# Performance work log

Hardware: AMD Instinct MI355X
Metric: run time of the kernel (lower is better)

The kernel has to match this reference:

```python
import jax, jax.numpy as jnp
import numpy as np
from jax import lax

V, E, H, T, S = 100000, 256, 512, 9, 4096
HH = H // 2
START, STOP = 7, 8
NEG = -10000.0


def setup_inputs() -> dict:
    key = jax.random.key(0)
    ks = jax.random.split(key, 16)
    def n(k, shape, scale=0.1):
        return jax.random.normal(k, shape, jnp.float32) * scale
    sentence = jax.random.randint(ks[0], (S,), 0, V)
    embed = n(ks[1], (V, E), 1.0)
    w_ih_f = n(ks[2], (4 * HH, E)); w_hh_f = n(ks[3], (4 * HH, HH))
    b_ih_f = n(ks[4], (4 * HH,));   b_hh_f = n(ks[5], (4 * HH,))
    w_ih_b = n(ks[6], (4 * HH, E)); w_hh_b = n(ks[7], (4 * HH, HH))
    b_ih_b = n(ks[8], (4 * HH,));   b_hh_b = n(ks[9], (4 * HH,))
    h0 = n(ks[10], (2, HH), 1.0)  # init_hidden: randn (2,1,HH), batch squeezed
    c0 = n(ks[11], (2, HH), 1.0)
    W_out = n(ks[12], (T, H)); b_out = n(ks[13], (T,))
    transitions = jax.random.normal(ks[14], (T, T), jnp.float32)
    transitions = transitions.at[START, :].set(NEG).at[:, STOP].set(NEG)
    return dict(sentence=sentence, embed=embed,
                w_ih_f=w_ih_f, w_hh_f=w_hh_f, b_ih_f=b_ih_f, b_hh_f=b_hh_f,
                w_ih_b=w_ih_b, w_hh_b=w_hh_b, b_ih_b=b_ih_b, b_hh_b=b_hh_b,
                h0=h0, c0=c0, W_out=W_out, b_out=b_out, transitions=transitions)


def _lstm_dir(x_gates, h0, c0, w_hh):
    # x_gates: [S, 4*HH] = x @ w_ih.T + b_ih + b_hh (precomputed input part)
    def step(carry, xg):
        h, c = carry
        g = xg + h @ w_hh.T
        i, f, gg, o = jnp.split(g, 4)  # torch gate order: i, f, g, o
        i = jax.nn.sigmoid(i); f = jax.nn.sigmoid(f)
        gg = jnp.tanh(gg);     o = jax.nn.sigmoid(o)
        c = f * c + i * gg
        h = o * jnp.tanh(c)
        return (h, c), h
    _, hs = lax.scan(step, (h0, c0), x_gates)
    return hs  # [S, HH]


def reference(sentence, embed, w_ih_f, w_hh_f, b_ih_f, b_hh_f,
              w_ih_b, w_hh_b, b_ih_b, b_hh_b, h0, c0, W_out, b_out, transitions):
    x = embed[sentence]  # [S, E]
    # bidirectional LSTM, batch=1
    hf = _lstm_dir(x @ w_ih_f.T + b_ih_f + b_hh_f, h0[0], c0[0], w_hh_f)
    hb = _lstm_dir((x @ w_ih_b.T + b_ih_b + b_hh_b)[::-1], h0[1], c0[1], w_hh_b)[::-1]
    lstm_out = jnp.concatenate([hf, hb], axis=-1)          # [S, H]
    frames = lstm_out @ W_out.T + b_out                     # [S, T] emission scores

    # Viterbi-style decode (faithful: alpha updated by logsumexp, backpointers by argmax)
    alpha0 = jnp.full((T,), NEG, jnp.float32).at[START].set(0.0)
    def vstep(alpha, frame):
        smat = alpha[:, None] + frame[None, :] + transitions  # [T, T]
        bp = jnp.argmax(smat, axis=0)
        return jax.nn.logsumexp(smat, axis=0), bp
    alpha, bps = lax.scan(vstep, alpha0, frames)            # bps: [S, T]

    final = alpha + transitions[:, STOP]                     # [T]
    best = jnp.argmax(final)
    score = jax.nn.logsumexp(final)

    # backtrack over bps[1:] in reverse
    def bstep(tag, bp):
        nt = bp[tag]
        return nt, nt
    _, path_rev = lax.scan(bstep, best, bps[1:][::-1])
    tag_seq = jnp.concatenate([path_rev[::-1], best[None]])  # [S]
    return score, tag_seq
```

## Files before the change

kernel.cpp:

```cpp
#include <hip/hip_runtime.h>
#include <hip/hip_bf16.h>

#define SEQ   4096
#define EMB   256
#define HHID  256
#define G4    1024
#define NT    9
#define TSTART 7
#define TSTOP  8
#define NEGV  (-10000.0f)
#define POISON 0xAAAAAAAAu

#define WS_XG_F   0u
#define WS_XG_B   16777216u
#define WS_HF     33554432u
#define WS_HB     37748736u
#define WS_FRAMES 41943040u

__global__ __launch_bounds__(256) void xgate_kernel(
    const int* __restrict__ sentence, const float* __restrict__ embed,
    const float* __restrict__ w_ih_f, const float* __restrict__ b_ih_f,
    const float* __restrict__ b_hh_f,
    const float* __restrict__ w_ih_b, const float* __restrict__ b_ih_b,
    const float* __restrict__ b_hh_b,
    float* __restrict__ xg_f, float* __restrict__ xg_b)
{
    const int st  = blockIdx.x;
    const int dir = blockIdx.y;
    const float* w  = dir ? w_ih_b : w_ih_f;
    const float* bi = dir ? b_ih_b : b_ih_f;
    const float* bh = dir ? b_hh_b : b_hh_f;
    float* xg = dir ? xg_b : xg_f;
    const int t = threadIdx.x;

    __shared__ float x_t[EMB][16];
    for (int sl = 0; sl < 16; ++sl) {
        int s   = st * 16 + sl;
        int tok = sentence[s];
        x_t[t][sl] = embed[(size_t)tok * EMB + t];
    }
    __syncthreads();

    float acc[4][16];
    #pragma unroll
    for (int q = 0; q < 4; ++q)
        #pragma unroll
        for (int sl = 0; sl < 16; ++sl) acc[q][sl] = 0.f;

    #pragma unroll 4
    for (int e = 0; e < EMB; ++e) {
        float w0 = w[(size_t)(t        ) * EMB + e];
        float w1 = w[(size_t)(t + 256  ) * EMB + e];
        float w2 = w[(size_t)(t + 512  ) * EMB + e];
        float w3 = w[(size_t)(t + 768  ) * EMB + e];
        #pragma unroll
        for (int sl = 0; sl < 16; ++sl) {
            float xv = x_t[e][sl];
            acc[0][sl] += w0 * xv;
            acc[1][sl] += w1 * xv;
            acc[2][sl] += w2 * xv;
            acc[3][sl] += w3 * xv;
        }
    }

    #pragma unroll
    for (int q = 0; q < 4; ++q) {
        int g = t + 256 * q;
        float bb = bi[g] + bh[g];
        for (int sl = 0; sl < 16; ++sl) {
            xg[(size_t)(st * 16 + sl) * G4 + g] = acc[q][sl] + bb;
        }
    }
}

__global__ __launch_bounds__(256, 1) void lstm_kernel(
    const float* __restrict__ xg_f, const float* __restrict__ xg_b,
    const float* __restrict__ w_hh_f, const float* __restrict__ w_hh_b,
    const float* __restrict__ h0, const float* __restrict__ c0,
    float* __restrict__ hf, float* __restrict__ hb)
{
    const int bx    = blockIdx.x;
    const int dir   = bx >> 3;
    const int slice = bx & 7;
    const int t     = threadIdx.x;

    const float* xg   = dir ? xg_b  : xg_f;
    const float* w_hh = dir ? w_hh_b : w_hh_f;
    float* hout = dir ? hb : hf;

    __shared__ float h_lds[HHID];
    __shared__ float gbuf[128];

    const int lr   = t >> 1;
    const int half = t & 1;
    const int type = lr >> 5;
    const int ul   = lr & 31;
    const int unit = slice * 32 + ul;
    const int grow = type * HHID + unit;

    float w[128];
    #pragma unroll
    for (int j = 0; j < 128; ++j)
        w[j] = w_hh[(size_t)grow * HHID + half * 128 + j];
    #pragma unroll
    for (int j = 0; j < 128; ++j)
        asm volatile("" : "+v"(w[j]));

    float c_reg = 0.f;
    if (t < 32) c_reg = c0[dir * HHID + slice * 32 + t];

    for (int n = 0; n < SEQ; ++n) {
        const int s = dir ? (SEQ - 1 - n) : n;

        float xgi = 0.f, xgff = 0.f, xgg = 0.f, xgo = 0.f;
        if (t < 32) {
            const float* xb = xg + (size_t)s * G4 + slice * 32 + t;
            xgi  = xb[0];
            xgff = xb[256];
            xgg  = xb[512];
            xgo  = xb[768];
        }

        if (n == 0) {
            h_lds[t] = h0[dir * HHID + t];
        } else if (t < 64) {
            const int sp = dir ? (s + 1) : (s - 1);
            unsigned int* src = (unsigned int*)(hout + (size_t)sp * HHID) + t * 4;
            unsigned got = 0;
            float hv[4];
            while (got != 0xFu) {
                #pragma unroll
                for (int j = 0; j < 4; ++j) {
                    if (!((got >> j) & 1u)) {
                        unsigned v = __hip_atomic_load(src + j, __ATOMIC_RELAXED,
                                                       __HIP_MEMORY_SCOPE_AGENT);
                        if (v != POISON) {
                            hv[j] = __uint_as_float(v);
                            got |= 1u << j;
                        }
                    }
                }
            }
            #pragma unroll
            for (int j = 0; j < 4; ++j) h_lds[t * 4 + j] = hv[j];
        }
        __syncthreads();

        float acc = 0.f;
        const float4* hv4 = (const float4*)(h_lds + half * 128);
        #pragma unroll
        for (int j4 = 0; j4 < 32; ++j4) {
            float4 hv = hv4[j4];
            acc += w[j4 * 4 + 0] * hv.x;
            acc += w[j4 * 4 + 1] * hv.y;
            acc += w[j4 * 4 + 2] * hv.z;
            acc += w[j4 * 4 + 3] * hv.w;
        }
        acc += __shfl_xor(acc, 1);
        if (half == 0) gbuf[lr] = acc;
        __syncthreads();

        if (t < 32) {
            float gi = gbuf[t]      + xgi;
            float gf = gbuf[32 + t] + xgff;
            float gg = gbuf[64 + t] + xgg;
            float go = gbuf[96 + t] + xgo;
            float iv = 1.f / (1.f + __expf(-gi));
            float fv = 1.f / (1.f + __expf(-gf));
            float gv = 1.f - 2.f / (__expf(2.f * gg) + 1.f);
            float ov = 1.f / (1.f + __expf(-go));
            float c  = fv * c_reg + iv * gv;
            c_reg = c;
            float h  = ov * (1.f - 2.f / (__expf(2.f * c) + 1.f));
            unsigned int* dst = (unsigned int*)(hout + (size_t)s * HHID) + slice * 32 + t;
            __hip_atomic_store(dst, __float_as_uint(h), __ATOMIC_RELAXED,
                               __HIP_MEMORY_SCOPE_AGENT);
        }
    }
}

__global__ __launch_bounds__(256) void frames_kernel(
    const float* __restrict__ hf, const float* __restrict__ hb,
    const float* __restrict__ W_out, const float* __restrict__ b_out,
    float* __restrict__ frames)
{
    int o = blockIdx.x * 256 + threadIdx.x;
    if (o >= SEQ * NT) return;
    int s = o / NT;
    int j = o - s * NT;
    const float4* a0 = (const float4*)(hf + (size_t)s * HHID);
    const float4* a1 = (const float4*)(hb + (size_t)s * HHID);
    const float4* w0 = (const float4*)(W_out + (size_t)j * 512);
    const float4* w1 = w0 + 64;
    float acc = 0.f;
    #pragma unroll 8
    for (int i = 0; i < 64; ++i) {
        float4 a = a0[i], b = w0[i];
        acc += a.x * b.x + a.y * b.y + a.z * b.z + a.w * b.w;
        float4 c = a1[i], d = w1[i];
        acc += c.x * d.x + c.y * d.y + c.z * d.z + c.w * d.w;
    }
    frames[o] = acc + b_out[j];
}

__global__ __launch_bounds__(64) void crf_kernel(
    const float* __restrict__ frames, const float* __restrict__ trans,
    float* __restrict__ dout)
{
    __shared__ float fr[512 * NT];
    __shared__ unsigned char bpl[SEQ * NT];
    const int t = threadIdx.x;
    const int tc = (t < NT) ? t : 0;

    float trow[NT];
    #pragma unroll
    for (int i = 0; i < NT; ++i) trow[i] = 0.f;
    if (t < NT) {
        #pragma unroll
        for (int i = 0; i < NT; ++i) trow[i] = trans[i * NT + t];
    }
    float alpha = (t == TSTART) ? 0.f : NEGV;

    for (int chunk = 0; chunk < 8; ++chunk) {
        for (int idx = t; idx < 512 * NT; idx += 64)
            fr[idx] = frames[chunk * 512 * NT + idx];
        __syncthreads();

        for (int sl = 0; sl < 512; ++sl) {
            const int s = chunk * 512 + sl;
            float v[NT];
            #pragma unroll
            for (int i = 0; i < NT; ++i)
                v[i] = __shfl(alpha, i) + trow[i];
            float mx = v[0];
            int   am = 0;
            #pragma unroll
            for (int i = 1; i < NT; ++i)
                if (v[i] > mx) { mx = v[i]; am = i; }
            float sum = 0.f;
            #pragma unroll
            for (int i = 0; i < NT; ++i) sum += __expf(v[i] - mx);
            float anew = fr[sl * NT + tc] + mx + __logf(sum);
            if (t < NT) {
                bpl[s * NT + t] = (unsigned char)am;
                alpha = anew;
            }
        }
        __syncthreads();
    }

    float fin = NEGV;
    if (t < NT) fin = alpha + trans[t * NT + TSTOP];
    float f[NT];
    #pragma unroll
    for (int j = 0; j < NT; ++j) f[j] = __shfl(fin, j);

    if (t == 0) {
        float mx = f[0];
        int best = 0;
        #pragma unroll
        for (int j = 1; j < NT; ++j)
            if (f[j] > mx) { mx = f[j]; best = j; }
        float sum = 0.f;
        #pragma unroll
        for (int j = 0; j < NT; ++j) sum += __expf(f[j] - mx);
        dout[0] = mx + __logf(sum);

        int cur = best;
        dout[1 + SEQ - 1] = (float)cur;
        for (int s = SEQ - 2; s >= 0; --s) {
            cur = bpl[(s + 1) * NT + cur];
            dout[1 + s] = (float)cur;
        }
    }
}

extern "C" void kernel_launch(void* const* d_in, const int* in_sizes, int n_in,
                              void* d_out, int out_size, void* d_ws, size_t ws_size,
                              hipStream_t stream)
{
    const int*   sentence = (const int*)  d_in[0];
    const float* embed    = (const float*)d_in[1];
    const float* w_ih_f   = (const float*)d_in[2];
    const float* w_hh_f   = (const float*)d_in[3];
    const float* b_ih_f   = (const float*)d_in[4];
    const float* b_hh_f   = (const float*)d_in[5];
    const float* w_ih_b   = (const float*)d_in[6];
    const float* w_hh_b   = (const float*)d_in[7];
    const float* b_ih_b   = (const float*)d_in[8];
    const float* b_hh_b   = (const float*)d_in[9];
    const float* h0       = (const float*)d_in[10];
    const float* c0       = (const float*)d_in[11];
    const float* W_out    = (const float*)d_in[12];
    const float* b_out    = (const float*)d_in[13];
    const float* trans    = (const float*)d_in[14];

    float* out = (float*)d_out;
    char*  ws  = (char*)d_ws;

    float* xg_f   = (float*)(ws + WS_XG_F);
    float* xg_b   = (float*)(ws + WS_XG_B);
    float* hf     = (float*)(ws + WS_HF);
    float* hb     = (float*)(ws + WS_HB);
    float* frames = (float*)(ws + WS_FRAMES);

    hipMemsetAsync(hf, 0xAA, 2u * SEQ * HHID * sizeof(float), stream);

    xgate_kernel<<<dim3(256, 2), 256, 0, stream>>>(
        sentence, embed, w_ih_f, b_ih_f, b_hh_f, w_ih_b, b_ih_b, b_hh_b,
        xg_f, xg_b);

    lstm_kernel<<<16, 256, 0, stream>>>(
        xg_f, xg_b, w_hh_f, w_hh_b, h0, c0, hf, hb);

    frames_kernel<<<(SEQ * NT + 255) / 256, 256, 0, stream>>>(
        hf, hb, W_out, b_out, frames);

    crf_kernel<<<1, 64, 0, stream>>>(frames, trans, out);
}
```

Before: 10.20 ms.

## Restructure LSTM recurrence: per-unit 4-gate rows, shuffle reduction, double-buffered LDS

Each group of 8 threads now owns one hidden unit and computes all four gate dot products over a 32-wide slice, reducing them with xor shuffles instead of an LDS round trip. This drops the second __syncthreads per step. The hidden state is double-buffered in LDS, and each block writes its own h slice locally, so it only polls the other blocks' values, with every thread polling one element. Weights are kept in AGPRs via inline accvgpr writes and reads, which frees VGPRs but adds a read instruction per weight use.

```diff
diff --git a/kernel.cpp b/kernel.cpp
--- a/kernel.cpp
+++ b/kernel.cpp
@@ -83,88 +83,97 @@
     const int dir   = bx >> 3;
     const int slice = bx & 7;
     const int t     = threadIdx.x;
+    const int cb    = t & 7;
+    const int rb    = t >> 3;
+    const int unit  = slice * 32 + rb;
 
     const float* xg   = dir ? xg_b  : xg_f;
     const float* w_hh = dir ? w_hh_b : w_hh_f;
     float* hout = dir ? hb : hf;
 
-    __shared__ float h_lds[HHID];
-    __shared__ float gbuf[128];
-
-    const int lr   = t >> 1;
-    const int half = t & 1;
-    const int type = lr >> 5;
-    const int ul   = lr & 31;
-    const int unit = slice * 32 + ul;
-    const int grow = type * HHID + unit;
-
-    float w[128];
-    #pragma unroll
-    for (int j = 0; j < 128; ++j)
-        w[j] = w_hh[(size_t)grow * HHID + half * 128 + j];
-    #pragma unroll
-    for (int j = 0; j < 128; ++j)
-        asm volatile("" : "+v"(w[j]));
+    __shared__ float buf[2][HHID];
+
+    float wa[128];
+    #pragma unroll
+    for (int q = 0; q < 4; ++q) {
+        #pragma unroll
+        for (int j = 0; j < 32; ++j) {
+            float tmp = w_hh[(size_t)(q * HHID + unit) * HHID + cb * 32 + j];
+            asm volatile("v_accvgpr_write_b32 %0, %1"
+                         : "=a"(wa[q * 32 + j]) : "v"(tmp));
+        }
+    }
 
     float c_reg = 0.f;
-    if (t < 32) c_reg = c0[dir * HHID + slice * 32 + t];
+    if (cb == 0) c_reg = c0[dir * HHID + unit];
+
+    const bool own = (t >= slice * 32) && (t < slice * 32 + 32);
 
     for (int n = 0; n < SEQ; ++n) {
         const int s = dir ? (SEQ - 1 - n) : n;
 
-        float xgi = 0.f, xgff = 0.f, xgg = 0.f, xgo = 0.f;
-        if (t < 32) {
-            const float* xb = xg + (size_t)s * G4 + slice * 32 + t;
-            xgi  = xb[0];
-            xgff = xb[256];
-            xgg  = xb[512];
-            xgo  = xb[768];
+        float xg0 = 0.f, xg1 = 0.f, xg2 = 0.f, xg3 = 0.f;
+        if (cb == 0) {
+            const float* xb = xg + (size_t)s * G4 + unit;
+            xg0 = xb[0];
+            xg1 = xb[HHID];
+            xg2 = xb[2 * HHID];
+            xg3 = xb[3 * HHID];
         }
 
         if (n == 0) {
-            h_lds[t] = h0[dir * HHID + t];
-        } else if (t < 64) {
+            buf[0][t] = h0[dir * HHID + t];
+        } else if (!own) {
             const int sp = dir ? (s + 1) : (s - 1);
-            unsigned int* src = (unsigned int*)(hout + (size_t)sp * HHID) + t * 4;
-            unsigned got = 0;
-            float hv[4];
-            while (got != 0xFu) {
-                #pragma unroll
-                for (int j = 0; j < 4; ++j) {
-                    if (!((got >> j) & 1u)) {
-                        unsigned v = __hip_atomic_load(src + j, __ATOMIC_RELAXED,
-                                                       __HIP_MEMORY_SCOPE_AGENT);
-                        if (v != POISON) {
-                            hv[j] = __uint_as_float(v);
-                            got |= 1u << j;
-                        }
-                    }
-                }
+            const unsigned int* src =
+                (const unsigned int*)(hout + (size_t)sp * HHID) + t;
+            unsigned v;
+            do {
+                v = __hip_atomic_load(src, __ATOMIC_RELAXED,
+                                      __HIP_MEMORY_SCOPE_AGENT);
+            } while (v == POISON);
+            buf[n & 1][t] = __uint_as_float(v);
+        }
+        __syncthreads();
+
+        float a0 = 0.f, a1 = 0.f, a2 = 0.f, a3 = 0.f;
+        const float4* h4 = (const float4*)(&buf[n & 1][cb * 32]);
+        #pragma unroll
+        for (int j4 = 0; j4 < 8; ++j4) {
+            float4 hv = h4[j4];
+            #pragma unroll
+            for (int k = 0; k < 4; ++k) {
+                float hk = (k == 0) ? hv.x : (k == 1) ? hv.y
+                         : (k == 2) ? hv.z : hv.w;
+                float w0, w1, w2, w3;
+                asm volatile("v_accvgpr_read_b32 %0, %1"
+                             : "=v"(w0) : "a"(wa[0 * 32 + j4 * 4 + k]));
+                asm volatile("v_accvgpr_read_b32 %0, %1"
+                             : "=v"(w1) : "a"(wa[1 * 32 + j4 * 4 + k]));
+                asm volatile("v_accvgpr_read_b32 %0, %1"
+                             : "=v"(w2) : "a"(wa[2 * 32 + j4 * 4 + k]));
+                asm volatile("v_accvgpr_read_b32 %0, %1"
+                             : "=v"(w3) : "a"(wa[3 * 32 + j4 * 4 + k]));
+                a0 += w0 * hk;
+                a1 += w1 * hk;
+                a2 += w2 * hk;
+                a3 += w3 * hk;
             }
-            #pragma unroll
-            for (int j = 0; j < 4; ++j) h_lds[t * 4 + j] = hv[j];
-        }
-        __syncthreads();
-
-        float acc = 0.f;
-        const float4* hv4 = (const float4*)(h_lds + half * 128);
-        #pragma unroll
-        for (int j4 = 0; j4 < 32; ++j4) {
-            float4 hv = hv4[j4];
-            acc += w[j4 * 4 + 0] * hv.x;
-            acc += w[j4 * 4 + 1] * hv.y;
-            acc += w[j4 * 4 + 2] * hv.z;
-            acc += w[j4 * 4 + 3] * hv.w;
-        }
-        acc += __shfl_xor(acc, 1);
-        if (half == 0) gbuf[lr] = acc;
-        __syncthreads();
-
-        if (t < 32) {
-            float gi = gbuf[t]      + xgi;
-            float gf = gbuf[32 + t] + xgff;
-            float gg = gbuf[64 + t] + xgg;
-            float go = gbuf[96 + t] + xgo;
+        }
+
+        #pragma unroll
+        for (int m = 1; m <= 4; m <<= 1) {
+            a0 += __shfl_xor(a0, m);
+            a1 += __shfl_xor(a1, m);
+            a2 += __shfl_xor(a2, m);
+            a3 += __shfl_xor(a3, m);
+        }
+
+        if (cb == 0) {
+            float gi = a0 + xg0;
+            float gf = a1 + xg1;
+            float gg = a2 + xg2;
+            float go = a3 + xg3;
             float iv = 1.f / (1.f + __expf(-gi));
             float fv = 1.f / (1.f + __expf(-gf));
             float gv = 1.f - 2.f / (__expf(2.f * gg) + 1.f);
@@ -172,9 +181,11 @@
             float c  = fv * c_reg + iv * gv;
             c_reg = c;
             float h  = ov * (1.f - 2.f / (__expf(2.f * c) + 1.f));
-            unsigned int* dst = (unsigned int*)(hout + (size_t)s * HHID) + slice * 32 + t;
+            unsigned int* dst =
+                (unsigned int*)(hout + (size_t)s * HHID) + unit;
             __hip_atomic_store(dst, __float_as_uint(h), __ATOMIC_RELAXED,
                                __HIP_MEMORY_SCOPE_AGENT);
+            buf[(n + 1) & 1][unit] = h;
         }
     }
 }
```

Measured after the change: 9.920 ms. -2.8%, faster.
